# Performance work log

Hardware: AMD Instinct MI355X
Metric: run time of the kernel (lower is better)

## Reference

```python
import jax, jax.numpy as jnp
import numpy as np

N = 100000   # nodes
E = 1600000  # edges (avg degree 16)
F = 128      # input features
H = 64       # hidden_dim
C = 10       # num_classes
G = 128      # graphs in batch
EPS = 1e-5   # BatchNorm eps


def setup_inputs() -> dict:
    key = jax.random.key(0)
    ks = jax.random.split(key, 24)
    d = {}
    d['x'] = jax.random.normal(ks[0], (N, F), jnp.float32)
    d['edge_index'] = jax.random.randint(ks[1], (2, E), 0, N)
    d['batch'] = jnp.sort(jax.random.randint(ks[2], (N,), 0, G))
    # SAGEConv1: lin_l (aggregated, with bias) + lin_r (root, no bias)
    d['W1l'] = jax.random.normal(ks[3], (F, H), jnp.float32) * 0.05
    d['W1r'] = jax.random.normal(ks[4], (F, H), jnp.float32) * 0.05
    d['b1'] = jnp.zeros((H,), jnp.float32)
    # SAGEConv2
    d['W2l'] = jax.random.normal(ks[5], (H, H), jnp.float32) * 0.1
    d['W2r'] = jax.random.normal(ks[6], (H, H), jnp.float32) * 0.1
    d['b2'] = jnp.zeros((H,), jnp.float32)
    # BatchNorm (eval mode: running stats)
    for i, (kg, kb, km, kv) in enumerate([(7, 8, 9, 10), (11, 12, 13, 14), (15, 16, 17, 18)], 1):
        d[f'bn{i}_g'] = jax.random.uniform(ks[kg], (H,), jnp.float32, 0.5, 1.5)
        d[f'bn{i}_b'] = jax.random.normal(ks[kb], (H,), jnp.float32) * 0.1
        d[f'bn{i}_m'] = jax.random.normal(ks[km], (H,), jnp.float32) * 0.1
        d[f'bn{i}_v'] = jax.random.uniform(ks[kv], (H,), jnp.float32, 0.5, 1.5)
    # classifier head
    d['Wc1'] = jax.random.normal(ks[19], (H, H), jnp.float32) * 0.1
    d['bc1'] = jnp.zeros((H,), jnp.float32)
    d['Wc2'] = jax.random.normal(ks[20], (H, C), jnp.float32) * 0.1
    d['bc2'] = jnp.zeros((C,), jnp.float32)
    return d


def _bn(x, g, b, m, v):
    return (x - m) * jax.lax.rsqrt(v + EPS) * g + b


def _sage(x, src, dst, Wl, Wr, b):
    # mean aggregation of source-node features at destination nodes
    msum = jax.ops.segment_sum(x[src], dst, num_segments=N)          # [N, d]
    cnt = jax.ops.segment_sum(jnp.ones((E,), x.dtype), dst, num_segments=N)
    mean = msum / jnp.maximum(cnt, 1.0)[:, None]
    return mean @ Wl + b + x @ Wr


def reference(x, edge_index, batch,
              W1l, W1r, b1, W2l, W2r, b2,
              bn1_g, bn1_b, bn1_m, bn1_v,
              bn2_g, bn2_b, bn2_m, bn2_v,
              Wc1, bc1, bn3_g, bn3_b, bn3_m, bn3_v,
              Wc2, bc2):
    src, dst = edge_index[0], edge_index[1]
    h = _sage(x, src, dst, W1l, W1r, b1)
    h = jax.nn.relu(_bn(h, bn1_g, bn1_b, bn1_m, bn1_v))
    h = _sage(h, src, dst, W2l, W2r, b2)
    h = jax.nn.relu(_bn(h, bn2_g, bn2_b, bn2_m, bn2_v))
    # global mean pool over graphs
    gsum = jax.ops.segment_sum(h, batch, num_segments=G)             # [G, H]
    gcnt = jax.ops.segment_sum(jnp.ones((N,), h.dtype), batch, num_segments=G)
    g = gsum / jnp.maximum(gcnt, 1.0)[:, None]
    # classifier head (eval: dropout is identity)
    g = jax.nn.relu(_bn(g @ Wc1 + bc1, bn3_g, bn3_b, bn3_m, bn3_v))
    logits = g @ Wc2 + bc2
    return jax.nn.log_softmax(logits, axis=1)
```

## Files before the change

### kernel.cpp

```cpp
#include <hip/hip_runtime.h>
#include <hip/hip_bf16.h>
#include <math.h>

#define NN 100000
#define NE 1600000
#define FF 128
#define HH 64
#define CC 10
#define GG 128
#define BN_EPS 1e-5f

#define BNODES 64
#define NB 1563
#define PBLK 128
#define ECHUNK 12500
#define MHIST (NB * PBLK)
#define NSCAN 782
#define SCOL_CAP 2048

#define PNODES 16
#define POOL_BLOCKS 1563

typedef short v8bf __attribute__((ext_vector_type(8)));
typedef float v4f  __attribute__((ext_vector_type(4)));

__device__ inline ushort f2b(float x) {
    __hip_bfloat16 h = __float2bfloat16(x);
    return *reinterpret_cast<ushort*>(&h);
}
__device__ inline float b2f(ushort u) {
    return __uint_as_float(((unsigned)u) << 16);
}
__device__ inline float blo(unsigned u) { return __uint_as_float(u << 16); }
__device__ inline float bhi(unsigned u) { return __uint_as_float(u & 0xffff0000u); }

template<int K>
__global__ __launch_bounds__(256) void w_swizzle(const float* __restrict__ Wl,
                                                 const float* __restrict__ Wr,
                                                 ushort* __restrict__ ol,
                                                 ushort* __restrict__ orr) {
    constexpr int T = (K / 32) * 4 * 64;
    const int t = blockIdx.x * 256 + threadIdx.x;
    if (t >= T) return;
    const int lane = t & 63, nt = (t >> 6) & 3, ks = t >> 8;
    const int m = lane & 15, quad = lane >> 4;
#pragma unroll
    for (int j = 0; j < 8; ++j) {
        const int kk = ks * 32 + quad * 8 + j;
        const int cc = nt * 16 + m;
        ol[t * 8 + j]  = f2b(Wl[kk * 64 + cc]);
        orr[t * 8 + j] = f2b(Wr[kk * 64 + cc]);
    }
}

template<int K, int TPB, bool AF32>
__global__ __launch_bounds__(256) void gemm_mfma(const void* __restrict__ Xv,
                                                 const ushort* __restrict__ Bl,
                                                 const ushort* __restrict__ Br,
                                                 ushort* __restrict__ Yl,
                                                 ushort* __restrict__ Yr) {
    constexpr int KS = K / 32;
    const int lane  = threadIdx.x & 63;
    const int wave  = threadIdx.x >> 6;
    const int nhalf = wave & 1;
    const int rsub  = wave >> 1;
    const int m = lane & 15, quad = lane >> 4;

    v8bf bl[KS][2], br[KS][2];
#pragma unroll
    for (int ks = 0; ks < KS; ++ks)
#pragma unroll
        for (int nt = 0; nt < 2; ++nt) {
            const int nti = nhalf * 2 + nt;
            bl[ks][nt] = *(const v8bf*)(Bl + ((size_t)(ks * 4 + nti) * 64 + lane) * 8);
            br[ks][nt] = *(const v8bf*)(Br + ((size_t)(ks * 4 + nti) * 64 + lane) * 8);
        }

    for (int it = 0; it < TPB; ++it) {
        const int bt = blockIdx.x * TPB + it;
        const int row0 = bt * 32 + rsub * 16;
        if (row0 >= NN) return;
        const v4f z = {0.f, 0.f, 0.f, 0.f};
        v4f accl[2] = {z, z}, accr[2] = {z, z};
#pragma unroll
        for (int ks = 0; ks < KS; ++ks) {
            v8bf a;
            if (AF32) {
                const float* xrow = (const float*)Xv + (size_t)(row0 + m) * K + quad * 8 + ks * 32;
                const float4 a0 = *(const float4*)(xrow);
                const float4 a1 = *(const float4*)(xrow + 4);
                a[0] = (short)f2b(a0.x); a[1] = (short)f2b(a0.y);
                a[2] = (short)f2b(a0.z); a[3] = (short)f2b(a0.w);
                a[4] = (short)f2b(a1.x); a[5] = (short)f2b(a1.y);
                a[6] = (short)f2b(a1.z); a[7] = (short)f2b(a1.w);
            } else {
                const ushort* xrow = (const ushort*)Xv + (size_t)(row0 + m) * K + quad * 8 + ks * 32;
                a = *(const v8bf*)xrow;
            }
#pragma unroll
            for (int nt = 0; nt < 2; ++nt) {
                accl[nt] = __builtin_amdgcn_mfma_f32_16x16x32_bf16(a, bl[ks][nt], accl[nt], 0, 0, 0);
                accr[nt] = __builtin_amdgcn_mfma_f32_16x16x32_bf16(a, br[ks][nt], accr[nt], 0, 0, 0);
            }
        }
#pragma unroll
        for (int nt = 0; nt < 2; ++nt) {
            const int cc = nhalf * 32 + nt * 16 + m;
#pragma unroll
            for (int r = 0; r < 4; ++r) {
                const size_t off = (size_t)(row0 + quad * 4 + r) * 64 + cc;
                Yl[off] = f2b(accl[nt][r]);
                Yr[off] = f2b(accr[nt][r]);
            }
        }
    }
}

__global__ __launch_bounds__(1024) void edge_hist(const int* __restrict__ dst,
                                                  int* __restrict__ hist) {
    __shared__ int h[NB];
    for (int i = threadIdx.x; i < NB; i += 1024) h[i] = 0;
    __syncthreads();
    const int e0 = blockIdx.x * ECHUNK;
    for (int e = e0 + threadIdx.x; e < e0 + ECHUNK; e += 1024)
        atomicAdd(&h[dst[e] >> 6], 1);
    __syncthreads();
    for (int i = threadIdx.x; i < NB; i += 1024)
        hist[i * PBLK + blockIdx.x] = h[i];
}

__global__ __launch_bounds__(256) void scan_block(const int* __restrict__ cnt,
                                                  int* __restrict__ rp,
                                                  int* __restrict__ bsum) {
    __shared__ int s[256];
    const int tid = threadIdx.x;
    const int i = blockIdx.x * 256 + tid;
    const int v = (i < MHIST) ? cnt[i] : 0;
    s[tid] = v;
    __syncthreads();
    for (int off = 1; off < 256; off <<= 1) {
        int t = (tid >= off) ? s[tid - off] : 0;
        __syncthreads();
        s[tid] += t;
        __syncthreads();
    }
    if (i < MHIST) rp[i] = s[tid] - v;
    if (tid == 255) bsum[blockIdx.x] = s[255];
}

__global__ __launch_bounds__(256) void scan_bsums(const int* __restrict__ bsum,
                                                  int* __restrict__ boff,
                                                  int* __restrict__ rp) {
    __shared__ int s[256];
    const int tid = threadIdx.x;
    int v[4];
    int tot = 0;
#pragma unroll
    for (int j = 0; j < 4; ++j) {
        const int idx = tid * 4 + j;
        v[j] = (idx < NSCAN) ? bsum[idx] : 0;
        tot += v[j];
    }
    s[tid] = tot;
    __syncthreads();
    for (int off = 1; off < 256; off <<= 1) {
        int t = (tid >= off) ? s[tid - off] : 0;
        __syncthreads();
        s[tid] += t;
        __syncthreads();
    }
    int run = s[tid] - tot;
#pragma unroll
    for (int j = 0; j < 4; ++j) {
        const int idx = tid * 4 + j;
        if (idx < NSCAN) boff[idx] = run;
        run += v[j];
    }
    if (tid == 0) rp[MHIST] = NE;
}

__global__ __launch_bounds__(256) void scan_add(int* __restrict__ rp,
                                                const int* __restrict__ boff) {
    const int i = blockIdx.x * 256 + threadIdx.x;
    if (i < MHIST) rp[i] += boff[blockIdx.x];
}

__global__ __launch_bounds__(1024) void edge_scatter(const int* __restrict__ src,
                                                     const int* __restrict__ dst,
                                                     const int* __restrict__ goffs,
                                                     int* __restrict__ pairs) {
    __shared__ int cur[NB];
    for (int i = threadIdx.x; i < NB; i += 1024)
        cur[i] = goffs[i * PBLK + blockIdx.x];
    __syncthreads();
    const int e0 = blockIdx.x * ECHUNK;
    for (int e = e0 + threadIdx.x; e < e0 + ECHUNK; e += 1024) {
        const int s = src[e];
        const int d = dst[e];
        const int pos = atomicAdd(&cur[d >> 6], 1);
        pairs[pos] = (s << 6) | (d & (BNODES - 1));
    }
}

__global__ __launch_bounds__(256) void spmm_sorted(const int* __restrict__ goffs,
                                                   const int* __restrict__ pairs,
                                                   const ushort* __restrict__ Yl,
                                                   const ushort* __restrict__ Yr,
                                                   const float* __restrict__ bias,
                                                   const float* __restrict__ bng,
                                                   const float* __restrict__ bnb,
                                                   const float* __restrict__ bnm,
                                                   const float* __restrict__ bnv,
                                                   ushort* __restrict__ outp) {
    __shared__ int scol[SCOL_CAP];
    __shared__ int deg[BNODES];
    __shared__ int loffs[BNODES];
    __shared__ int fill[BNODES];
    const int tid = threadIdx.x;
    const int b = blockIdx.x;

    if (tid < BNODES) { deg[tid] = 0; fill[tid] = 0; }
    __syncthreads();

    const int beg = goffs[b * PBLK];
    int end = goffs[(b + 1) * PBLK];
    if (end - beg > SCOL_CAP) end = beg + SCOL_CAP;

    for (int i = beg + tid; i < end; i += 256)
        atomicAdd(&deg[pairs[i] & (BNODES - 1)], 1);
    __syncthreads();

    if (tid < BNODES) loffs[tid] = deg[tid];
    __syncthreads();
    for (int s = 1; s < BNODES; s <<= 1) {
        int v = 0;
        if (tid < BNODES && tid >= s) v = loffs[tid - s];
        __syncthreads();
        if (tid < BNODES) loffs[tid] += v;
        __syncthreads();
    }

    for (int i = beg + tid; i < end; i += 256) {
        const int pv = pairs[i];
        const int dl = pv & (BNODES - 1);
        const int pos = (loffs[dl] - deg[dl]) + atomicAdd(&fill[dl], 1);
        scol[pos] = pv >> 6;
    }
    __syncthreads();

    const int wv = tid >> 6, lane = tid & 63;
    const int grp = lane >> 4, subl = lane & 15;

    const float4 bias4 = *(const float4*)(bias + subl * 4);
    const float4 g4 = *(const float4*)(bng + subl * 4);
    const float4 v4 = *(const float4*)(bnv + subl * 4);
    const float4 m4 = *(const float4*)(bnm + subl * 4);
    const float4 bb4 = *(const float4*)(bnb + subl * 4);
    const float sc0 = g4.x * rsqrtf(v4.x + BN_EPS);
    const float sc1 = g4.y * rsqrtf(v4.y + BN_EPS);
    const float sc2 = g4.z * rsqrtf(v4.z + BN_EPS);
    const float sc3 = g4.w * rsqrtf(v4.w + BN_EPS);

    for (int i = 0; i < 4; ++i) {
        const int nl = wv * 16 + i * 4 + grp;
        const int node = b * BNODES + nl;
        if (node >= NN) continue;
        const int dg = deg[nl];
        const int nbeg = loffs[nl] - dg;
        const int nend = nbeg + dg;
        float a0 = 0.f, a1 = 0.f, a2 = 0.f, a3 = 0.f;
        float c0 = 0.f, c1 = 0.f, c2 = 0.f, c3 = 0.f;
        int e = nbeg;
        for (; e + 1 < nend; e += 2) {
            const int s0 = scol[e];
            const int s1 = scol[e + 1];
            const uint2 r0 = *(const uint2*)(Yl + (size_t)s0 * 64 + subl * 4);
            const uint2 r1 = *(const uint2*)(Yl + (size_t)s1 * 64 + subl * 4);
            a0 += blo(r0.x); a1 += bhi(r0.x); a2 += blo(r0.y); a3 += bhi(r0.y);
            c0 += blo(r1.x); c1 += bhi(r1.x); c2 += blo(r1.y); c3 += bhi(r1.y);
        }
        if (e < nend) {
            const int s0 = scol[e];
            const uint2 r0 = *(const uint2*)(Yl + (size_t)s0 * 64 + subl * 4);
            a0 += blo(r0.x); a1 += bhi(r0.x); a2 += blo(r0.y); a3 += bhi(r0.y);
        }
        a0 += c0; a1 += c1; a2 += c2; a3 += c3;
        const float inv = 1.0f / fmaxf((float)dg, 1.0f);
        const uint2 yr = *(const uint2*)(Yr + (size_t)node * 64 + subl * 4);
        const float h0 = a0 * inv + bias4.x + blo(yr.x);
        const float h1 = a1 * inv + bias4.y + bhi(yr.x);
        const float h2 = a2 * inv + bias4.z + blo(yr.y);
        const float h3 = a3 * inv + bias4.w + bhi(yr.y);
        const float o0 = fmaxf((h0 - m4.x) * sc0 + bb4.x, 0.0f);
        const float o1 = fmaxf((h1 - m4.y) * sc1 + bb4.y, 0.0f);
        const float o2 = fmaxf((h2 - m4.z) * sc2 + bb4.z, 0.0f);
        const float o3 = fmaxf((h3 - m4.w) * sc3 + bb4.w, 0.0f);
        uint2 o;
        o.x = (unsigned)f2b(o0) | ((unsigned)f2b(o1) << 16);
        o.y = (unsigned)f2b(o2) | ((unsigned)f2b(o3) << 16);
        *(uint2*)(outp + (size_t)node * 64 + subl * 4) = o;
    }
}

__global__ __launch_bounds__(256) void pool_seg(const ushort* __restrict__ h,
                                                const int* __restrict__ batch,
                                                float* __restrict__ gsum,
                                                float* __restrict__ gcnt) {
    const int wave = blockIdx.x * 4 + (threadIdx.x >> 6);
    const int lane = threadIdx.x & 63;
    const int n0 = wave * PNODES;
    if (n0 >= NN) return;
    const int n1 = (n0 + PNODES < NN) ? n0 + PNODES : NN;
    int g = batch[n0];
    float acc = 0.f, c = 0.f;
#pragma unroll 4
    for (int n = n0; n < n1; ++n) {
        const int b = batch[n];
        if (b != g) {
            atomicAdd(&gsum[g * 64 + lane], acc);
            if (lane == 0) atomicAdd(&gcnt[g], c);
            acc = 0.f; c = 0.f; g = b;
        }
        acc += b2f(h[(size_t)n * 64 + lane]);
        c += 1.0f;
    }
    atomicAdd(&gsum[g * 64 + lane], acc);
    if (lane == 0) atomicAdd(&gcnt[g], c);
}

__global__ __launch_bounds__(64) void head_kernel(const float* __restrict__ gsum,
                                                  const float* __restrict__ gcnt,
                                                  const float* __restrict__ Wc1,
                                                  const float* __restrict__ bc1,
                                                  const float* __restrict__ g3,
                                                  const float* __restrict__ b3,
                                                  const float* __restrict__ m3,
                                                  const float* __restrict__ v3,
                                                  const float* __restrict__ Wc2,
                                                  const float* __restrict__ bc2,
                                                  float* __restrict__ out) {
    __shared__ float sg[64];
    __shared__ float st[64];
    __shared__ float sl[10];
    __shared__ float sls;
    const int b = blockIdx.x;
    const int c = threadIdx.x;
    sg[c] = gsum[b * 64 + c] / fmaxf(gcnt[b], 1.0f);
    __syncthreads();
    float acc = bc1[c];
#pragma unroll
    for (int k = 0; k < 64; ++k) acc += sg[k] * Wc1[k * 64 + c];
    const float sc = g3[c] * rsqrtf(v3[c] + BN_EPS);
    st[c] = fmaxf((acc - m3[c]) * sc + b3[c], 0.0f);
    __syncthreads();
    if (c < CC) {
        float lg = bc2[c];
#pragma unroll
        for (int k = 0; k < 64; ++k) lg += st[k] * Wc2[k * CC + c];
        sl[c] = lg;
    }
    __syncthreads();
    if (c == 0) {
        float mx = sl[0];
        for (int i = 1; i < CC; ++i) mx = fmaxf(mx, sl[i]);
        float s = 0.f;
        for (int i = 0; i < CC; ++i) s += expf(sl[i] - mx);
        sls = mx + logf(s);
    }
    __syncthreads();
    if (c < CC) out[b * CC + c] = sl[c] - sls;
}

extern "C" void kernel_launch(void* const* d_in, const int* in_sizes, int n_in,
                              void* d_out, int out_size, void* d_ws, size_t ws_size,
                              hipStream_t stream) {
    const float* x    = (const float*)d_in[0];
    const int*   ei   = (const int*)d_in[1];
    const int*   batch= (const int*)d_in[2];
    const float* W1l  = (const float*)d_in[3];
    const float* W1r  = (const float*)d_in[4];
    const float* b1   = (const float*)d_in[5];
    const float* W2l  = (const float*)d_in[6];
    const float* W2r  = (const float*)d_in[7];
    const float* b2   = (const float*)d_in[8];
    const float* bn1g = (const float*)d_in[9];
    const float* bn1b = (const float*)d_in[10];
    const float* bn1m = (const float*)d_in[11];
    const float* bn1v = (const float*)d_in[12];
    const float* bn2g = (const float*)d_in[13];
    const float* bn2b = (const float*)d_in[14];
    const float* bn2m = (const float*)d_in[15];
    const float* bn2v = (const float*)d_in[16];
    const float* bn3g = (const float*)d_in[17];
    const float* bn3b = (const float*)d_in[18];
    const float* bn3m = (const float*)d_in[19];
    const float* bn3v = (const float*)d_in[20];
    const float* Wc1  = (const float*)d_in[21];
    const float* bc1  = (const float*)d_in[22];
    const float* Wc2  = (const float*)d_in[23];
    const float* bc2  = (const float*)d_in[24];
    float* out = (float*)d_out;

    const int* src = ei;
    const int* dst = ei + NE;

    char* p = (char*)d_ws;
    ushort* yl   = (ushort*)p;                 p += (size_t)NN * 64 * 2;
    ushort* yr   = (ushort*)p;                 p += (size_t)NN * 64 * 2;
    ushort* hbuf = (ushort*)p;                 p += (size_t)NN * 64 * 2;
    int*    pairs= (int*)p;                    p += (size_t)NE * 4;
    int*    hist = (int*)p;                    p += (size_t)MHIST * 4;
    int*    goffs= (int*)p;                    p += (size_t)(MHIST + 1) * 4;
    int*    bsum = (int*)p;                    p += 1024 * 4;
    int*    boff = (int*)p;                    p += 1024 * 4;
    ushort* w1ls = (ushort*)p;                 p += (size_t)FF * 64 * 2;
    ushort* w1rs = (ushort*)p;                 p += (size_t)FF * 64 * 2;
    ushort* w2ls = (ushort*)p;                 p += (size_t)HH * 64 * 2;
    ushort* w2rs = (ushort*)p;                 p += (size_t)HH * 64 * 2;
    float* gsum  = (float*)p;                  p += (size_t)GG * 64 * 4;
    float* gcnt  = (float*)p;                  p += (size_t)GG * 4;

    edge_hist<<<PBLK, 1024, 0, stream>>>(dst, hist);
    scan_block<<<NSCAN, 256, 0, stream>>>(hist, goffs, bsum);
    scan_bsums<<<1, 256, 0, stream>>>(bsum, boff, goffs);
    scan_add<<<NSCAN, 256, 0, stream>>>(goffs, boff);
    edge_scatter<<<PBLK, 1024, 0, stream>>>(src, dst, goffs, pairs);

    w_swizzle<FF><<<((FF / 32) * 256 + 255) / 256, 256, 0, stream>>>(W1l, W1r, w1ls, w1rs);
    w_swizzle<HH><<<((HH / 32) * 256 + 255) / 256, 256, 0, stream>>>(W2l, W2r, w2ls, w2rs);

    gemm_mfma<FF, 2, true><<<1563, 256, 0, stream>>>((const void*)x, w1ls, w1rs, yl, yr);
    spmm_sorted<<<NB, 256, 0, stream>>>(goffs, pairs, yl, yr, b1,
                                        bn1g, bn1b, bn1m, bn1v, hbuf);

    gemm_mfma<HH, 2, false><<<1563, 256, 0, stream>>>((const void*)hbuf, w2ls, w2rs, yl, yr);
    spmm_sorted<<<NB, 256, 0, stream>>>(goffs, pairs, yl, yr, b2,
                                        bn2g, bn2b, bn2m, bn2v, hbuf);

    hipMemsetAsync(gsum, 0, (size_t)(GG * 64 + GG) * sizeof(float), stream);
    pool_seg<<<POOL_BLOCKS, 256, 0, stream>>>(hbuf, batch, gsum, gcnt);
    head_kernel<<<GG, 64, 0, stream>>>(gsum, gcnt, Wc1, bc1,
                                       bn3g, bn3b, bn3m, bn3v, Wc2, bc2, out);
}
```

Baseline: 307.0 us.

## Fold scan_add into consumers, merge prep launches, widen SpMM gather to 16B

Removes the scan_add pass by having edge_scatter and spmm_sorted add block offsets on the fly. Merges the two weight-swizzle launches and the pooling memset into one prep kernel. Caches pair values in registers to avoid a second global read. Switches the SpMM gather to 8 channels per lane with 16-byte loads, 8 nodes per wave-iteration. Fewer launches and wider gathers, at some cost in register pressure. The fixed pv[8] buffer assumes at most 8 pairs per thread, which holds given the SCOL_CAP clamp.

After: 289.4 us. 5.7% less time.

```diff
diff --git a/kernel.cpp b/kernel.cpp
--- a/kernel.cpp
+++ b/kernel.cpp
@@ -34,22 +34,36 @@
 __device__ inline float blo(unsigned u) { return __uint_as_float(u << 16); }
 __device__ inline float bhi(unsigned u) { return __uint_as_float(u & 0xffff0000u); }
 
-template<int K>
-__global__ __launch_bounds__(256) void w_swizzle(const float* __restrict__ Wl,
-                                                 const float* __restrict__ Wr,
-                                                 ushort* __restrict__ ol,
-                                                 ushort* __restrict__ orr) {
-    constexpr int T = (K / 32) * 4 * 64;
-    const int t = blockIdx.x * 256 + threadIdx.x;
-    if (t >= T) return;
+__device__ inline void sw_one(const float* __restrict__ W, ushort* __restrict__ o,
+                              int t, int K) {
     const int lane = t & 63, nt = (t >> 6) & 3, ks = t >> 8;
     const int m = lane & 15, quad = lane >> 4;
 #pragma unroll
     for (int j = 0; j < 8; ++j) {
         const int kk = ks * 32 + quad * 8 + j;
         const int cc = nt * 16 + m;
-        ol[t * 8 + j]  = f2b(Wl[kk * 64 + cc]);
-        orr[t * 8 + j] = f2b(Wr[kk * 64 + cc]);
+        o[t * 8 + j] = f2b(W[kk * 64 + cc]);
+    }
+}
+
+__global__ __launch_bounds__(256) void prep_kernel(const float* __restrict__ W1l,
+                                                   const float* __restrict__ W1r,
+                                                   const float* __restrict__ W2l,
+                                                   const float* __restrict__ W2r,
+                                                   ushort* __restrict__ w1ls,
+                                                   ushort* __restrict__ w1rs,
+                                                   ushort* __restrict__ w2ls,
+                                                   ushort* __restrict__ w2rs,
+                                                   float* __restrict__ gz) {
+    const int t = blockIdx.x * 256 + threadIdx.x;
+    if (t < 1024) {
+        sw_one(W1l, w1ls, t, FF);
+        sw_one(W1r, w1rs, t, FF);
+    } else if (t < 1536) {
+        sw_one(W2l, w2ls, t - 1024, HH);
+        sw_one(W2r, w2rs, t - 1024, HH);
+    } else {
+        for (int i = t - 1536; i < GG * 64 + GG; i += 512) gz[i] = 0.f;
     }
 }
 
@@ -149,8 +163,7 @@
 }
 
 __global__ __launch_bounds__(256) void scan_bsums(const int* __restrict__ bsum,
-                                                  int* __restrict__ boff,
-                                                  int* __restrict__ rp) {
+                                                  int* __restrict__ boff) {
     __shared__ int s[256];
     const int tid = threadIdx.x;
     int v[4];
@@ -176,22 +189,18 @@
         if (idx < NSCAN) boff[idx] = run;
         run += v[j];
     }
-    if (tid == 0) rp[MHIST] = NE;
-}
-
-__global__ __launch_bounds__(256) void scan_add(int* __restrict__ rp,
-                                                const int* __restrict__ boff) {
-    const int i = blockIdx.x * 256 + threadIdx.x;
-    if (i < MHIST) rp[i] += boff[blockIdx.x];
 }
 
 __global__ __launch_bounds__(1024) void edge_scatter(const int* __restrict__ src,
                                                      const int* __restrict__ dst,
                                                      const int* __restrict__ goffs,
+                                                     const int* __restrict__ boff,
                                                      int* __restrict__ pairs) {
     __shared__ int cur[NB];
-    for (int i = threadIdx.x; i < NB; i += 1024)
-        cur[i] = goffs[i * PBLK + blockIdx.x];
+    for (int i = threadIdx.x; i < NB; i += 1024) {
+        const int idx = i * PBLK + blockIdx.x;
+        cur[i] = goffs[idx] + boff[idx >> 8];
+    }
     __syncthreads();
     const int e0 = blockIdx.x * ECHUNK;
     for (int e = e0 + threadIdx.x; e < e0 + ECHUNK; e += 1024) {
@@ -203,6 +212,7 @@
 }
 
 __global__ __launch_bounds__(256) void spmm_sorted(const int* __restrict__ goffs,
+                                                   const int* __restrict__ boff,
                                                    const int* __restrict__ pairs,
                                                    const ushort* __restrict__ Yl,
                                                    const ushort* __restrict__ Yr,
@@ -222,12 +232,17 @@
     if (tid < BNODES) { deg[tid] = 0; fill[tid] = 0; }
     __syncthreads();
 
-    const int beg = goffs[b * PBLK];
-    int end = goffs[(b + 1) * PBLK];
+    const int beg = goffs[b * PBLK] + boff[b >> 1];
+    int end = (b == NB - 1) ? NE : goffs[(b + 1) * PBLK] + boff[(b + 1) >> 1];
     if (end - beg > SCOL_CAP) end = beg + SCOL_CAP;
 
-    for (int i = beg + tid; i < end; i += 256)
-        atomicAdd(&deg[pairs[i] & (BNODES - 1)], 1);
+    int pv[8];
+    int npv = 0;
+    for (int i = beg + tid; i < end; i += 256) {
+        const int v = pairs[i];
+        pv[npv++] = v;
+        atomicAdd(&deg[v & (BNODES - 1)], 1);
+    }
     __syncthreads();
 
     if (tid < BNODES) loffs[tid] = deg[tid];
@@ -240,65 +255,74 @@
         __syncthreads();
     }
 
-    for (int i = beg + tid; i < end; i += 256) {
-        const int pv = pairs[i];
-        const int dl = pv & (BNODES - 1);
+    for (int j = 0; j < npv; ++j) {
+        const int v = pv[j];
+        const int dl = v & (BNODES - 1);
         const int pos = (loffs[dl] - deg[dl]) + atomicAdd(&fill[dl], 1);
-        scol[pos] = pv >> 6;
+        scol[pos] = v >> 6;
     }
     __syncthreads();
 
     const int wv = tid >> 6, lane = tid & 63;
-    const int grp = lane >> 4, subl = lane & 15;
-
-    const float4 bias4 = *(const float4*)(bias + subl * 4);
-    const float4 g4 = *(const float4*)(bng + subl * 4);
-    const float4 v4 = *(const float4*)(bnv + subl * 4);
-    const float4 m4 = *(const float4*)(bnm + subl * 4);
-    const float4 bb4 = *(const float4*)(bnb + subl * 4);
-    const float sc0 = g4.x * rsqrtf(v4.x + BN_EPS);
-    const float sc1 = g4.y * rsqrtf(v4.y + BN_EPS);
-    const float sc2 = g4.z * rsqrtf(v4.z + BN_EPS);
-    const float sc3 = g4.w * rsqrtf(v4.w + BN_EPS);
-
-    for (int i = 0; i < 4; ++i) {
-        const int nl = wv * 16 + i * 4 + grp;
+    const int grp = lane >> 3, subl = lane & 7;
+
+    float biasj[8], scj[8], mj[8], bbj[8];
+#pragma unroll
+    for (int j = 0; j < 8; ++j) {
+        const int ch = subl * 8 + j;
+        biasj[j] = bias[ch];
+        scj[j] = bng[ch] * rsqrtf(bnv[ch] + BN_EPS);
+        mj[j] = bnm[ch];
+        bbj[j] = bnb[ch];
+    }
+
+    for (int i = 0; i < 2; ++i) {
+        const int nl = wv * 16 + i * 8 + grp;
         const int node = b * BNODES + nl;
         if (node >= NN) continue;
         const int dg = deg[nl];
         const int nbeg = loffs[nl] - dg;
         const int nend = nbeg + dg;
-        float a0 = 0.f, a1 = 0.f, a2 = 0.f, a3 = 0.f;
-        float c0 = 0.f, c1 = 0.f, c2 = 0.f, c3 = 0.f;
+        float a[8] = {0.f, 0.f, 0.f, 0.f, 0.f, 0.f, 0.f, 0.f};
+        float c[8] = {0.f, 0.f, 0.f, 0.f, 0.f, 0.f, 0.f, 0.f};
         int e = nbeg;
         for (; e + 1 < nend; e += 2) {
             const int s0 = scol[e];
             const int s1 = scol[e + 1];
-            const uint2 r0 = *(const uint2*)(Yl + (size_t)s0 * 64 + subl * 4);
-            const uint2 r1 = *(const uint2*)(Yl + (size_t)s1 * 64 + subl * 4);
-            a0 += blo(r0.x); a1 += bhi(r0.x); a2 += blo(r0.y); a3 += bhi(r0.y);
-            c0 += blo(r1.x); c1 += bhi(r1.x); c2 += blo(r1.y); c3 += bhi(r1.y);
+            const uint4 r0 = *(const uint4*)(Yl + (size_t)s0 * 64 + subl * 8);
+            const uint4 r1 = *(const uint4*)(Yl + (size_t)s1 * 64 + subl * 8);
+            a[0] += blo(r0.x); a[1] += bhi(r0.x); a[2] += blo(r0.y); a[3] += bhi(r0.y);
+            a[4] += blo(r0.z); a[5] += bhi(r0.z); a[6] += blo(r0.w); a[7] += bhi(r0.w);
+            c[0] += blo(r1.x); c[1] += bhi(r1.x); c[2] += blo(r1.y); c[3] += bhi(r1.y);
+            c[4] += blo(r1.z); c[5] += bhi(r1.z); c[6] += blo(r1.w); c[7] += bhi(r1.w);
         }
         if (e < nend) {
             const int s0 = scol[e];
-            const uint2 r0 = *(const uint2*)(Yl + (size_t)s0 * 64 + subl * 4);
-            a0 += blo(r0.x); a1 += bhi(r0.x); a2 += blo(r0.y); a3 += bhi(r0.y);
-        }
-        a0 += c0; a1 += c1; a2 += c2; a3 += c3;
+            const uint4 r0 = *(const uint4*)(Yl + (size_t)s0 * 64 + subl * 8);
+            a[0] += blo(r0.x); a[1] += bhi(r0.x); a[2] += blo(r0.y); a[3] += bhi(r0.y);
+            a[4] += blo(r0.z); a[5] += bhi(r0.z); a[6] += blo(r0.w); a[7] += bhi(r0.w);
+        }
         const float inv = 1.0f / fmaxf((float)dg, 1.0f);
-        const uint2 yr = *(const uint2*)(Yr + (size_t)node * 64 + subl * 4);
-        const float h0 = a0 * inv + bias4.x + blo(yr.x);
-        const float h1 = a1 * inv + bias4.y + bhi(yr.x);
-        const float h2 = a2 * inv + bias4.z + blo(yr.y);
-        const float h3 = a3 * inv + bias4.w + bhi(yr.y);
-        const float o0 = fmaxf((h0 - m4.x) * sc0 + bb4.x, 0.0f);
-        const float o1 = fmaxf((h1 - m4.y) * sc1 + bb4.y, 0.0f);
-        const float o2 = fmaxf((h2 - m4.z) * sc2 + bb4.z, 0.0f);
-        const float o3 = fmaxf((h3 - m4.w) * sc3 + bb4.w, 0.0f);
-        uint2 o;
-        o.x = (unsigned)f2b(o0) | ((unsigned)f2b(o1) << 16);
-        o.y = (unsigned)f2b(o2) | ((unsigned)f2b(o3) << 16);
-        *(uint2*)(outp + (size_t)node * 64 + subl * 4) = o;
+        const uint4 yr = *(const uint4*)(Yr + (size_t)node * 64 + subl * 8);
+        float hj[8];
+        hj[0] = (a[0] + c[0]) * inv + biasj[0] + blo(yr.x);
+        hj[1] = (a[1] + c[1]) * inv + biasj[1] + bhi(yr.x);
+        hj[2] = (a[2] + c[2]) * inv + biasj[2] + blo(yr.y);
+        hj[3] = (a[3] + c[3]) * inv + biasj[3] + bhi(yr.y);
+        hj[4] = (a[4] + c[4]) * inv + biasj[4] + blo(yr.z);
+        hj[5] = (a[5] + c[5]) * inv + biasj[5] + bhi(yr.z);
+        hj[6] = (a[6] + c[6]) * inv + biasj[6] + blo(yr.w);
+        hj[7] = (a[7] + c[7]) * inv + biasj[7] + bhi(yr.w);
+        unsigned ow[4];
+#pragma unroll
+        for (int j = 0; j < 4; ++j) {
+            const float o0 = fmaxf((hj[2 * j] - mj[2 * j]) * scj[2 * j] + bbj[2 * j], 0.0f);
+            const float o1 = fmaxf((hj[2 * j + 1] - mj[2 * j + 1]) * scj[2 * j + 1] + bbj[2 * j + 1], 0.0f);
+            ow[j] = (unsigned)f2b(o0) | ((unsigned)f2b(o1) << 16);
+        }
+        uint4 o;
+        o.x = ow[0]; o.y = ow[1]; o.z = ow[2]; o.w = ow[3];
+        *(uint4*)(outp + (size_t)node * 64 + subl * 8) = o;
     }
 }
 
@@ -410,7 +434,7 @@
     ushort* hbuf = (ushort*)p;                 p += (size_t)NN * 64 * 2;
     int*    pairs= (int*)p;                    p += (size_t)NE * 4;
     int*    hist = (int*)p;                    p += (size_t)MHIST * 4;
-    int*    goffs= (int*)p;                    p += (size_t)(MHIST + 1) * 4;
+    int*    goffs= (int*)p;                    p += (size_t)MHIST * 4;
     int*    bsum = (int*)p;                    p += 1024 * 4;
     int*    boff = (int*)p;                    p += 1024 * 4;
     ushort* w1ls = (ushort*)p;                 p += (size_t)FF * 64 * 2;
@@ -418,26 +442,23 @@
     ushort* w2ls = (ushort*)p;                 p += (size_t)HH * 64 * 2;
     ushort* w2rs = (ushort*)p;                 p += (size_t)HH * 64 * 2;
     float* gsum  = (float*)p;                  p += (size_t)GG * 64 * 4;
-    float* gcnt  = (float*)p;                  p += (size_t)GG * 4;
+    float* gcnt  = gsum + GG * 64;             p += (size_t)GG * 4;
 
     edge_hist<<<PBLK, 1024, 0, stream>>>(dst, hist);
     scan_block<<<NSCAN, 256, 0, stream>>>(hist, goffs, bsum);
-    scan_bsums<<<1, 256, 0, stream>>>(bsum, boff, goffs);
-    scan_add<<<NSCAN, 256, 0, stream>>>(goffs, boff);
-    edge_scatter<<<PBLK, 1024, 0, stream>>>(src, dst, goffs, pairs);
-
-    w_swizzle<FF><<<((FF / 32) * 256 + 255) / 256, 256, 0, stream>>>(W1l, W1r, w1ls, w1rs);
-    w_swizzle<HH><<<((HH / 32) * 256 + 255) / 256, 256, 0, stream>>>(W2l, W2r, w2ls, w2rs);
+    scan_bsums<<<1, 256, 0, stream>>>(bsum, boff);
+    edge_scatter<<<PBLK, 1024, 0, stream>>>(src, dst, goffs, boff, pairs);
+
+    prep_kernel<<<8, 256, 0, stream>>>(W1l, W1r, W2l, W2r, w1ls, w1rs, w2ls, w2rs, gsum);
 
     gemm_mfma<FF, 2, true><<<1563, 256, 0, stream>>>((const void*)x, w1ls, w1rs, yl, yr);
-    spmm_sorted<<<NB, 256, 0, stream>>>(goffs, pairs, yl, yr, b1,
+    spmm_sorted<<<NB, 256, 0, stream>>>(goffs, boff, pairs, yl, yr, b1,
                                         bn1g, bn1b, bn1m, bn1v, hbuf);
 
     gemm_mfma<HH, 2, false><<<1563, 256, 0, stream>>>((const void*)hbuf, w2ls, w2rs, yl, yr);
-    spmm_sorted<<<NB, 256, 0, stream>>>(goffs, pairs, yl, yr, b2,
+    spmm_sorted<<<NB, 256, 0, stream>>>(goffs, boff, pairs, yl, yr, b2,
                                         bn2g, bn2b, bn2m, bn2v, hbuf);
 
-    hipMemsetAsync(gsum, 0, (size_t)(GG * 64 + GG) * sizeof(float), stream);
     pool_seg<<<POOL_BLOCKS, 256, 0, stream>>>(hbuf, batch, gsum, gcnt);
     head_kernel<<<GG, 64, 0, stream>>>(gsum, gcnt, Wc1, bc1,
                                        bn3g, bn3b, bn3m, bn3v, Wc2, bc2, out);
```
